# Kernel tuning notes

Measured on AMD Instinct MI355X. Metric: run time of the kernel, lower is better.

## Reference

```python
import jax, jax.numpy as jnp
import numpy as np

DIM = 512; HEADS = 8; DH = 64; INNER = HEADS * DH
GAMMA = 0.01; LREG = 1e-3
QB = 16; NS = 512


def _ln(x, g, b):
    mu = x.mean(-1, keepdims=True)
    var = jnp.var(x, axis=-1, keepdims=True)  # biased, matches torch LayerNorm
    return (x - mu) / jnp.sqrt(var + 1e-5) * g + b


def _std(x):
    return jnp.std(x, ddof=1)  # torch.std default is unbiased


def setup_inputs() -> dict:
    key = jax.random.key(0)
    ks = jax.random.split(key, 10)
    sc = lambda k, shape: (jax.random.normal(k, shape, jnp.float32) * 0.05)
    return {
        "q": jax.random.normal(ks[0], (QB, NS, DIM), jnp.float32),
        "k": jax.random.normal(ks[1], (QB, NS, DIM), jnp.float32),
        "v": jax.random.normal(ks[2], (QB, NS, DIM), jnp.float32),
        "ln1_g": jnp.ones((DIM,), jnp.float32),
        "ln1_b": jnp.zeros((DIM,), jnp.float32),
        "W_in": sc(ks[3], (DIM, INNER)),
        "wp_w1": sc(ks[4], (2 * DH, 2 * DH)),
        "wp_b1": jnp.zeros((2 * DH,), jnp.float32),
        "wp_ln_g": jnp.ones((2 * DH,), jnp.float32),
        "wp_ln_b": jnp.zeros((2 * DH,), jnp.float32),
        "wp_w2": sc(ks[5], (2 * DH, DH)),
        "wp_b2": jnp.zeros((DH,), jnp.float32),
        "wp_w3": sc(ks[6], (DH, 3)),
        "wp_b3": jnp.zeros((3,), jnp.float32),
        "weight_temp": jnp.array([0.5], jnp.float32),
        "W_out": sc(ks[7], (INNER, DIM)),
        "b_out": jnp.zeros((DIM,), jnp.float32),
    }


def _forward(q, k, v, ln1_g, ln1_b, W_in, wp_w1, wp_b1, wp_ln_g, wp_ln_b,
             wp_w2, wp_b2, wp_w3, wp_b3, weight_temp, W_out, b_out):
    eps = 1e-6

    def proj(t):  # LayerNorm -> Linear(no bias) -> [h, q, n, d]
        y = _ln(t, ln1_g, ln1_b) @ W_in
        Qb, Nb, _ = y.shape
        return y.reshape(Qb, Nb, HEADS, DH).transpose(2, 0, 1, 3)

    f_q, f_k, f_v = proj(q), proj(k), proj(v)
    m = f_k.shape[2]

    # --- cosine distance component ---
    dots_raw = jnp.einsum('hqnd,hqmd->hqnm', f_q, f_k)
    n1 = jnp.linalg.norm(f_q, axis=-1, keepdims=True) + eps          # [h,q,n,1]
    n2 = jnp.linalg.norm(f_k, axis=-1)[:, :, None, :] + eps          # [h,q,1,m]
    cosine_sim = jnp.clip(dots_raw / (n1 * n2), -0.9, 0.9)

    # --- regularized covariance component ---
    fkc = f_k - f_k.mean(axis=2, keepdims=True)   # center keys over n
    fqc = f_q - f_q.mean(axis=-1, keepdims=True)  # center queries over d
    cov = jnp.einsum('hqnd,hqmd->hqnm', fqc, fkc) / (DH ** 0.5 + 1e-6)
    cov = jnp.clip((LREG / max(m, 1)) * cov, -10.0, 10.0)

    # --- margin-based variance component (eval: adaptive_gamma = gamma) ---
    fqn = f_q / jnp.maximum(jnp.linalg.norm(f_q, axis=-1, keepdims=True), 1e-6)
    fkn = f_k / jnp.maximum(jnp.linalg.norm(f_k, axis=-1, keepdims=True), 1e-6)
    cs = jnp.clip(jnp.einsum('hqnd,hqmd->hqnm', fqn, fkn), -0.9, 0.9)
    margin = jnp.clip(GAMMA - cs, 0.0, 5.0)
    var_comp = jnp.broadcast_to(margin.mean(-1, keepdims=True), cs.shape)

    # --- dynamic per-head mixture weights ---
    feat = jnp.concatenate([f_q.mean((1, 2)), f_k.mean((1, 2))], axis=-1)  # [h, 2d]
    x = jax.nn.relu(_ln(feat @ wp_w1 + wp_b1, wp_ln_g, wp_ln_b))
    x = jax.nn.relu(x @ wp_w2 + wp_b2)
    wlog = jax.nn.softmax(x @ wp_w3 + wp_b3, axis=-1)  # predictor ends in Softmax
    wt = jnp.clip(weight_temp, 0.1, 2.0)
    w = jax.nn.softmax(wlog / wt, axis=-1)             # second softmax over temp
    w = jnp.clip(w, 0.05, 0.8)
    w = w / w.sum(-1, keepdims=True)
    cos_w = w[:, 0].reshape(HEADS, 1, 1, 1)
    cov_w = w[:, 1].reshape(HEADS, 1, 1, 1)
    var_w = w[:, 2].reshape(HEADS, 1, 1, 1)

    sg = jax.lax.stop_gradient  # norms are .detach()'d in torch
    dots = (cos_w * (cosine_sim / (sg(_std(cosine_sim)) + 1e-6))
            + cov_w * (cov / (sg(_std(cov)) + 1e-6) * 0.5)
            + var_w * (var_comp / (sg(_std(var_comp)) + 1e-6) * 0.5))

    ds = _std(dots)
    temp = jnp.where(ds < 1e-4, jnp.float32(0.1),
                     jnp.where(ds < 0.01, jnp.float32(0.3), 0.5 + ds))
    temp = jnp.clip(temp, 0.1, 3.0)

    attn = jax.nn.softmax(dots / temp, axis=-1)
    out = jnp.einsum('hqnm,hqmd->hqnd', attn, f_v)
    out = out.transpose(1, 2, 0, 3).reshape(q.shape[0], q.shape[1], INNER)
    return out @ W_out + b_out


def reference(q, k, v, ln1_g, ln1_b, W_in, wp_w1, wp_b1, wp_ln_g, wp_ln_b,
              wp_w2, wp_b2, wp_w3, wp_b3, weight_temp, W_out, b_out):
    return _forward(q, k, v, ln1_g, ln1_b, W_in, wp_w1, wp_b1, wp_ln_g,
                    wp_ln_b, wp_w2, wp_b2, wp_w3, wp_b3, weight_temp,
                    W_out, b_out)
```

## Files before the change

### kernel.cpp

```cpp
#include <hip/hip_runtime.h>
#include <math.h>

#define H 8
#define NS 512
#define D 64

typedef __bf16 bf16x8 __attribute__((ext_vector_type(8)));
typedef _Float16 f16x8 __attribute__((ext_vector_type(8)));
typedef float f32x4 __attribute__((ext_vector_type(4)));
typedef short s16x8 __attribute__((ext_vector_type(8)));
typedef short s16x4 __attribute__((ext_vector_type(4)));

#define CS2 ((1e-3f/512.f)/(8.f+1e-6f))
#define LOG2E 1.4426950408889634

static __device__ __forceinline__ f32x4 mfma16(bf16x8 a, bf16x8 b, f32x4 c){
  return __builtin_amdgcn_mfma_f32_16x16x32_bf16(a,b,c,0,0,0);
}
static __device__ __forceinline__ f32x4 mfma16h(f16x8 a, f16x8 b, f32x4 c){
  return __builtin_amdgcn_mfma_f32_16x16x32_f16(a,b,c,0,0,0);
}
static __device__ __forceinline__ float b2f(unsigned short s){
  union { unsigned u; float f; } v; v.u = ((unsigned)s)<<16; return v.f;
}
static __device__ __forceinline__ unsigned short f2b(float f){
  union { float f; unsigned u; } v; v.f = f;
  unsigned r = v.u + 0x7FFFu + ((v.u>>16)&1u);
  return (unsigned short)(r>>16);
}
static __device__ __forceinline__ unsigned short f2h(float f){
  union { _Float16 h; unsigned short s; } cv; cv.h = (_Float16)f; return cv.s;
}
static __device__ __forceinline__ float h2f(unsigned short s){
  union { _Float16 h; unsigned short s; } cv; cv.s = s; return (float)cv.h;
}
static __device__ __forceinline__ float wred64(float v){
  #pragma unroll
  for(int m=32; m>0; m>>=1) v += __shfl_xor(v, m, 64);
  return v;
}

constexpr size_t OFF_XNB = 0;
constexpr size_t OFF_FQB = 6291456;
constexpr size_t OFF_FKB = 8388608;
constexpr size_t OFF_FVB = 10485760;
constexpr size_t OFF_FVT = 12582912;
constexpr size_t OFF_WT  = 14680064;
constexpr size_t OFF_WOH = 14811136;
constexpr size_t OFF_WOL = 14942208;
constexpr size_t OFF_OHH = 15073280;
constexpr size_t OFF_ARR = 19267584;
constexpr size_t OFF_SMK = OFF_ARR + 9*65536;
constexpr size_t OFF_COEF= OFF_SMK + 128;
constexpr size_t OFF_DBL = OFF_COEF + 32;
constexpr size_t NDBL    = 72 + 1024;

__global__ __launch_bounds__(256) void k_pre(const float* __restrict__ q,
    const float* __restrict__ k, const float* __restrict__ v,
    const float* __restrict__ g, const float* __restrict__ b,
    const float* __restrict__ Win, const float* __restrict__ Wout,
    unsigned short* __restrict__ xnb, unsigned short* __restrict__ WT,
    unsigned short* __restrict__ WTh, unsigned short* __restrict__ WTl,
    double* __restrict__ dbl){
  int bx = blockIdx.x; int t = threadIdx.x;
  if(bx < 6144){
    int row = bx*4 + (t>>6); int l = t & 63;
    const float* src = (row < 8192) ? q : ((row < 16384) ? k : v);
    int r = row & 8191;
    const float4* sp = (const float4*)(src + (size_t)r*512);
    float4 v1 = sp[l*2], v2 = sp[l*2+1];
    float s  = v1.x+v1.y+v1.z+v1.w + v2.x+v2.y+v2.z+v2.w;
    float ss = v1.x*v1.x+v1.y*v1.y+v1.z*v1.z+v1.w*v1.w
             + v2.x*v2.x+v2.y*v2.y+v2.z*v2.z+v2.w*v2.w;
    s = wred64(s); ss = wred64(ss);
    float mu = s*(1.f/512.f);
    float var = ss*(1.f/512.f) - mu*mu;
    float rstd = rsqrtf(var + 1e-5f);
    const float4* gp = (const float4*)g; const float4* bp = (const float4*)b;
    float4 g1 = gp[l*2], g2 = gp[l*2+1], b1 = bp[l*2], b2 = bp[l*2+1];
    s16x8 o;
    o[0]=(short)f2b((v1.x-mu)*rstd*g1.x+b1.x); o[1]=(short)f2b((v1.y-mu)*rstd*g1.y+b1.y);
    o[2]=(short)f2b((v1.z-mu)*rstd*g1.z+b1.z); o[3]=(short)f2b((v1.w-mu)*rstd*g1.w+b1.w);
    o[4]=(short)f2b((v2.x-mu)*rstd*g2.x+b2.x); o[5]=(short)f2b((v2.y-mu)*rstd*g2.y+b2.y);
    o[6]=(short)f2b((v2.z-mu)*rstd*g2.z+b2.z); o[7]=(short)f2b((v2.w-mu)*rstd*g2.w+b2.w);
    *(s16x8*)(xnb + (size_t)row*512 + l*8) = o;
    return;
  }
  __shared__ float tile[64][65];
  if(bx < 6208){
    int bb = bx - 6144; int kt = bb>>3, nt = bb&7;
    if(bb==0){
      for(int i=t;i<(int)NDBL;i+=256) dbl[i]=0.0;
    }
    #pragma unroll
    for(int i=0;i<4;i++){
      int row = (t>>4) + i*16; int col = (t&15)*4;
      float4 vv = *(const float4*)(Win + (size_t)(kt*64+row)*512 + nt*64 + col);
      tile[row][col]=vv.x; tile[row][col+1]=vv.y; tile[row][col+2]=vv.z; tile[row][col+3]=vv.w;
    }
    __syncthreads();
    #pragma unroll
    for(int i=0;i<4;i++){
      int n = (t>>4) + i*16; int ck = (t&15)*4;
      s16x4 o;
      #pragma unroll
      for(int j=0;j<4;j++) o[j] = (short)f2b(tile[ck+j][n]);
      *(s16x4*)(WT + (size_t)(nt*64+n)*512 + kt*64 + ck) = o;
    }
  } else {
    int bb = bx - 6208; int kt = bb>>3, nt = bb&7;
    #pragma unroll
    for(int i=0;i<4;i++){
      int row = (t>>4) + i*16; int col = (t&15)*4;
      float4 vv = *(const float4*)(Wout + (size_t)(kt*64+row)*512 + nt*64 + col);
      tile[row][col]=vv.x; tile[row][col+1]=vv.y; tile[row][col+2]=vv.z; tile[row][col+3]=vv.w;
    }
    __syncthreads();
    #pragma unroll
    for(int i=0;i<4;i++){
      int n = (t>>4) + i*16; int ck = (t&15)*4;
      s16x4 oh_, ol_;
      #pragma unroll
      for(int j=0;j<4;j++){
        float x = tile[ck+j][n];
        unsigned short hi = f2h(x);
        oh_[j] = (short)hi;
        ol_[j] = (short)f2h(x - h2f(hi));
      }
      *(s16x4*)(WTh + (size_t)(nt*64+n)*512 + kt*64 + ck) = oh_;
      *(s16x4*)(WTl + (size_t)(nt*64+n)*512 + kt*64 + ck) = ol_;
    }
  }
}

__global__ __launch_bounds__(256) void k_mm1(const unsigned short* __restrict__ xnb,
    const unsigned short* __restrict__ WT,
    unsigned short* __restrict__ fqb, unsigned short* __restrict__ fkb,
    unsigned short* __restrict__ fvb){
  __shared__ __align__(16) unsigned short As[128*64];
  __shared__ __align__(16) unsigned short Bs[128*64];
  int t = threadIdx.x; int w = t>>6; int l = t&63; int g = l>>4, lc = l&15;
  int bid = blockIdx.x;
  int work = (bid&7)*96 + (bid>>3);
  int Rb = (work>>2)*128, cb = (work&3)*128;
  int wr = (w>>1)*64, wc = (w&1)*64;
  f32x4 acc[4][4];
  #pragma unroll
  for(int i=0;i<4;i++)
    #pragma unroll
    for(int j=0;j<4;j++) acc[i][j] = (f32x4){0.f,0.f,0.f,0.f};
  for(int k0=0; k0<512; k0+=64){
    __syncthreads();
    #pragma unroll
    for(int i=0;i<4;i++){
      int c = t + i*256; int row = c>>3, k8 = c&7;
      s16x8 va = *(const s16x8*)(xnb + (size_t)(Rb+row)*512 + k0 + k8*8);
      *(s16x8*)((char*)As + row*128 + ((k8*16) ^ ((row&7)<<4))) = va;
      s16x8 vb = *(const s16x8*)(WT + (size_t)(cb+row)*512 + k0 + k8*8);
      *(s16x8*)((char*)Bs + row*128 + ((k8*16) ^ ((row&7)<<4))) = vb;
    }
    __syncthreads();
    #pragma unroll
    for(int ks=0; ks<2; ks++){
      bf16x8 ar[4], br[4];
      #pragma unroll
      for(int rt=0; rt<4; rt++){
        int row = wr + rt*16 + lc;
        ar[rt] = *(const bf16x8*)((const char*)As + row*128 + (((ks*4+g)*16) ^ ((row&7)<<4)));
      }
      #pragma unroll
      for(int ct=0; ct<4; ct++){
        int row = wc + ct*16 + lc;
        br[ct] = *(const bf16x8*)((const char*)Bs + row*128 + (((ks*4+g)*16) ^ ((row&7)<<4)));
      }
      #pragma unroll
      for(int rt=0; rt<4; rt++)
        #pragma unroll
        for(int ct=0; ct<4; ct++)
          acc[rt][ct] = mfma16(ar[rt], br[ct], acc[rt][ct]);
    }
  }
  #pragma unroll
  for(int rt=0; rt<4; rt++){
    #pragma unroll
    for(int r=0; r<4; r++){
      int R = Rb + wr + rt*16 + g*4 + r;
      int tsel = R>>13; int rr = R&8191;
      unsigned short* dst = (tsel==0)?fqb:((tsel==1)?fkb:fvb);
      #pragma unroll
      for(int ct=0; ct<4; ct++){
        int c = cb + wc + ct*16 + lc;
        dst[(size_t)rr*512 + c] = f2b(acc[rt][ct][r]);
      }
    }
  }
}

__global__ __launch_bounds__(512) void k_mid(const unsigned short* __restrict__ fqb,
    const unsigned short* __restrict__ fkb, const unsigned short* __restrict__ fvb,
    float* __restrict__ smk, double* featd,
    float* __restrict__ ri1, float* __restrict__ mq, float* __restrict__ qdm,
    float* __restrict__ ri2, float* __restrict__ sk,
    unsigned short* __restrict__ fvT){
  int bx = blockIdx.x; int t = threadIdx.x;
  if(bx < 128){
    int hq = bx; int h = hq>>4, q = hq&15;
    __shared__ float cq[8][64], ck[8][64], mkS[64];
    __shared__ float smkS;
    {
      int d = t&63; int g = t>>6;
      float aq=0.f, ak=0.f;
      for(int n=g; n<512; n+=8){
        size_t base = (size_t)(q*512+n)*512 + h*64 + d;
        aq += b2f(fqb[base]);
        ak += b2f(fkb[base]);
      }
      cq[g][d]=aq; ck[g][d]=ak;
    }
    __syncthreads();
    if(t<64){
      float sq=0.f, sk2=0.f;
      #pragma unroll
      for(int i=0;i<8;i++){ sq+=cq[i][t]; sk2+=ck[i][t]; }
      atomicAdd(&featd[h*128+t], (double)sq);
      atomicAdd(&featd[h*128+64+t], (double)sk2);
      float mk = sk2*(1.f/512.f);
      mkS[t]=mk;
      float s = wred64(mk);
      if(t==0){ smk[hq]=s; smkS=s; }
    }
    __syncthreads();
    {
      int n = t;
      float smkv = smkS;
      const unsigned short* fr = fqb + (size_t)(q*512+n)*512 + h*64;
      const unsigned short* kr = fkb + (size_t)(q*512+n)*512 + h*64;
      float sq=0.f, ssq=0.f, dq=0.f, sks=0.f, ssk=0.f;
      #pragma unroll
      for(int j=0;j<8;j++){
        s16x8 vq = *(const s16x8*)(fr + j*8);
        s16x8 vk = *(const s16x8*)(kr + j*8);
        #pragma unroll
        for(int e=0;e<8;e++){
          float a = b2f((unsigned short)vq[e]);
          float c = b2f((unsigned short)vk[e]);
          sq += a; ssq += a*a; dq += a*mkS[j*8+e];
          sks += c; ssk += c*c;
        }
      }
      int idx = hq*512 + n;
      float nq = sqrtf(ssq);
      ri1[idx]  = 1.f/(nq+1e-6f);
      mq[idx]   = sq*(1.f/64.f);
      qdm[idx]  = dq;
      float nk = sqrtf(ssk);
      ri2[idx]  = 1.f/(nk+1e-6f);
      sk[idx]   = sks - smkv;
    }
    return;
  }
  {
    int bb = bx - 128; int hq = bb>>2, nc = bb&3;
    int h = hq>>4, q = hq&15; int n0 = nc*128;
    __shared__ float tile[128][65];
    #pragma unroll
    for(int i=0;i<2;i++){
      int c = t + i*512; int row = c>>3, k8 = c&7;
      s16x8 v = *(const s16x8*)(fvb + (size_t)(q*512 + n0 + row)*512 + h*64 + k8*8);
      #pragma unroll
      for(int j=0;j<8;j++) tile[row][k8*8+j] = b2f((unsigned short)v[j]);
    }
    __syncthreads();
    #pragma unroll
    for(int i=0;i<2;i++){
      int c = t + i*512; int d = c>>4, n8 = c&15;
      s16x8 o;
      #pragma unroll
      for(int j=0;j<8;j++){
        int p = n8*8+j;
        int pl = p & 31;
        int src = (p & ~31) | (16*(pl&1) + (pl>>1));
        o[j] = (short)f2h(tile[src][d]);
      }
      *(s16x8*)(fvT + (size_t)(hq*64 + d)*512 + n0 + n8*8) = o;
    }
  }
}

__global__ __launch_bounds__(512) void k_comp(const unsigned short* __restrict__ fqb,
    const unsigned short* __restrict__ fkb,
    const float* __restrict__ ri1,
    const float* __restrict__ mq, const float* __restrict__ qdm,
    const float* __restrict__ ri2,
    const float* __restrict__ skp,
    float* __restrict__ mxcg, float* __restrict__ mxvg, double* headsum){
  int bid = blockIdx.x;
  int bx = (bid&7)*64 + (bid>>3);
  int hq = bx>>2; int rt = bx&3;
  int h = hq>>4, q = hq&15; int n0 = rt*128;
  __shared__ __align__(16) unsigned short Qs[128*64];
  __shared__ __align__(16) unsigned short Ks[128*64];
  __shared__ float ri2f[512], skf[512];
  __shared__ float red[8][9];
  int t = threadIdx.x; int w = t>>6; int l = t&63; int g = l>>4, lc = l&15;
  for(int i=t; i<512; i+=512){
    ri2f[i]=ri2[hq*NS+i]; skf[i]=skp[hq*NS+i];
  }
  #pragma unroll
  for(int i=0;i<2;i++){
    int c = t + i*512; int row = c>>3, k8 = c&7;
    s16x8 v = *(const s16x8*)(fqb + (size_t)(q*512 + n0 + row)*512 + h*64 + k8*8);
    *(s16x8*)((char*)Qs + row*128 + ((k8*16) ^ ((row&7)<<4))) = v;
  }
  float ri1r[4], mqr[4], qdmr[4];
  #pragma unroll
  for(int r=0;r<4;r++){
    int n = hq*NS + n0 + w*16 + g*4 + r;
    ri1r[r]=ri1[n]; mqr[r]=mq[n]; qdmr[r]=qdm[n];
  }
  __syncthreads();
  bf16x8 aq[2];
  #pragma unroll
  for(int ks=0;ks<2;ks++){
    int row = 16*w + lc;
    aq[ks] = *(const bf16x8*)((const char*)Qs + row*128 + (((ks*4+g)*16) ^ ((row&7)<<4)));
  }
  float p1=0,p3=0,p4=0;
  float rm_m[4]={0,0,0,0}, rm_c[4]={0,0,0,0}, rm_v[4]={0,0,0,0};
  float mxc[4]={-1e30f,-1e30f,-1e30f,-1e30f}, mxv[4]={-1e30f,-1e30f,-1e30f,-1e30f};
  for(int mc=0; mc<4; mc++){
    __syncthreads();
    #pragma unroll
    for(int i=0;i<2;i++){
      int c = t + i*512; int row = c>>3, k8 = c&7;
      s16x8 v = *(const s16x8*)(fkb + (size_t)(q*512 + mc*128 + row)*512 + h*64 + k8*8);
      *(s16x8*)((char*)Ks + row*128 + ((k8*16) ^ ((row&7)<<4))) = v;
    }
    __syncthreads();
    #pragma unroll 2
    for(int mt=0; mt<8; mt++){
      f32x4 dacc = (f32x4){0.f,0.f,0.f,0.f};
      #pragma unroll
      for(int ks=0;ks<2;ks++){
        int row = mt*16 + lc;
        bf16x8 bk = *(const bf16x8*)((const char*)Ks + row*128 + (((ks*4+g)*16) ^ ((row&7)<<4)));
        dacc = mfma16(aq[ks], bk, dacc);
      }
      int m = mc*128 + mt*16 + lc;
      float r2 = ri2f[m], sc = skf[m];
      #pragma unroll
      for(int r=0;r<4;r++){
        float dv = dacc[r];
        float cosv = fminf(fmaxf(dv*ri1r[r]*r2, -0.9f), 0.9f);
        float inner = (dv - qdmr[r]) - mqr[r]*sc;
        float marg = fmaxf(0.01f - cosv, 0.f);
        p1 += cosv*cosv; p3 += inner*inner; p4 += cosv*inner;
        rm_m[r]+=marg; rm_c[r]+=cosv; rm_v[r]+=inner;
        mxc[r]=fmaxf(mxc[r],cosv); mxv[r]=fmaxf(mxv[r],inner);
      }
    }
  }
  float p0 = rm_c[0]+rm_c[1]+rm_c[2]+rm_c[3];
  float p2 = rm_v[0]+rm_v[1]+rm_v[2]+rm_v[3];
  #pragma unroll
  for(int off=1; off<16; off<<=1){
    #pragma unroll
    for(int r=0;r<4;r++){
      rm_m[r]+=__shfl_xor(rm_m[r],off,64);
      rm_c[r]+=__shfl_xor(rm_c[r],off,64);
      rm_v[r]+=__shfl_xor(rm_v[r],off,64);
      mxc[r]=fmaxf(mxc[r],__shfl_xor(mxc[r],off,64));
      mxv[r]=fmaxf(mxv[r],__shfl_xor(mxv[r],off,64));
    }
  }
  float q0=0,q1=0,q2=0,q3=0;
  if(lc==0){
    #pragma unroll
    for(int r=0;r<4;r++){
      float vmv = rm_m[r]*(1.f/512.f);
      q0+=vmv; q1+=vmv*vmv; q2+=vmv*rm_c[r]; q3+=vmv*rm_v[r];
      int n = n0 + w*16 + g*4 + r;
      mxcg[hq*NS+n]=mxc[r]; mxvg[hq*NS+n]=mxv[r];
    }
  }
  float all9[9] = {p0,p1,p2,p3,p4,q0,q1,q2,q3};
  #pragma unroll
  for(int j=0;j<9;j++){
    float vv = wred64(all9[j]);
    if(l==0) red[w][j]=vv;
  }
  __syncthreads();
  if(t<9){
    double s = 0.0;
    #pragma unroll
    for(int i=0;i<8;i++) s += (double)red[i][t];
    atomicAdd(&headsum[h*9+t], s);
  }
}

__global__ __launch_bounds__(512) void k_finalize(const double* headsum, const double* featd,
    const float* __restrict__ w1, const float* __restrict__ b1,
    const float* __restrict__ lng, const float* __restrict__ lnb,
    const float* __restrict__ w2, const float* __restrict__ b2,
    const float* __restrict__ w3, const float* __restrict__ b3,
    const float* __restrict__ wtemp, float* coef){
  __shared__ float fS[1024];
  __shared__ float x1[1024];
  __shared__ float x2[512];
  __shared__ float oS[8][3], whS[8][3];
  int t = threadIdx.x;
  fS[t]     = (float)(featd[t]     * (1.0/8192.0));
  fS[t+512] = (float)(featd[t+512] * (1.0/8192.0));
  __syncthreads();
  int hh = t>>6, j = t&63;
  {
    float a0 = b1[j], a1 = b1[j+64];
    #pragma unroll 8
    for(int i=0;i<128;i++){
      float f = fS[hh*128+i];
      a0 += f*w1[(size_t)i*128 + j];
      a1 += f*w1[(size_t)i*128 + j + 64];
    }
    float s = a0+a1, ss = a0*a0+a1*a1;
    s = wred64(s); ss = wred64(ss);
    float mu = s*(1.f/128.f), var = ss*(1.f/128.f)-mu*mu;
    float rstd = rsqrtf(var+1e-5f);
    x1[hh*128+j]    = fmaxf((a0-mu)*rstd*lng[j]+lnb[j], 0.f);
    x1[hh*128+j+64] = fmaxf((a1-mu)*rstd*lng[j+64]+lnb[j+64], 0.f);
  }
  __syncthreads();
  {
    float s2 = b2[j];
    #pragma unroll 8
    for(int i=0;i<128;i++) s2 += x1[hh*128+i]*w2[(size_t)i*64+j];
    x2[hh*64+j] = fmaxf(s2, 0.f);
  }
  __syncthreads();
  if(t < 24){
    int h3 = t/3, j3 = t-h3*3;
    float s3=0.f;
    #pragma unroll 8
    for(int i=0;i<64;i++) s3 += x2[h3*64+i]*w3[i*3+j3];
    oS[h3][j3] = s3 + b3[j3];
  }
  __syncthreads();
  if(t < 8){
    float o0=oS[t][0], o1=oS[t][1], o2=oS[t][2];
    float mx=fmaxf(o0,fmaxf(o1,o2));
    float e0=expf(o0-mx), e1=expf(o1-mx), e2=expf(o2-mx), se=e0+e1+e2;
    float l0=e0/se, l1=e1/se, l2=e2/se;
    float wt=fminf(fmaxf(wtemp[0],0.1f),2.0f);
    l0/=wt; l1/=wt; l2/=wt;
    mx=fmaxf(l0,fmaxf(l1,l2));
    e0=expf(l0-mx); e1=expf(l1-mx); e2=expf(l2-mx); se=e0+e1+e2;
    float u0=fminf(fmaxf(e0/se,0.05f),0.8f);
    float u1=fminf(fmaxf(e1/se,0.05f),0.8f);
    float u2=fminf(fmaxf(e2/se,0.05f),0.8f);
    float su=u0+u1+u2;
    whS[t][0]=u0/su; whS[t][1]=u1/su; whS[t][2]=u2/su;
  }
  __syncthreads();
  if(t==0){
    const double N = 33554432.0;
    const double CS2d = (double)CS2;
    double gs[9];
    for(int jj=0;jj<9;jj++){ double s=0; for(int h2=0;h2<8;h2++) s+=headsum[h2*9+jj]; gs[jj]=s; }
    auto sd = [&](double s, double ss)->double{
      double vv=(ss - s*s/N)/(N-1.0); return vv>0.0 ? sqrt(vv) : 0.0;
    };
    double std_cos = sd(gs[0],gs[1]);
    double std_cov = sd(CS2d*gs[2], CS2d*CS2d*gs[3]);
    double std_vm  = sd(512.0*gs[5], 512.0*gs[6]);
    double sdot=0.0, sdot2=0.0;
    double Af[8], Bf[8];
    for(int h2=0;h2<8;h2++){
      const double* hs = headsum + h2*9;
      double A = (double)whS[h2][0]/(std_cos+1e-6);
      double Bi = (double)whS[h2][1]/(std_cov+1e-6)*0.5*CS2d;
      double C = (double)whS[h2][2]/(std_vm +1e-6)*0.5;
      sdot  += A*hs[0] + Bi*hs[2] + C*512.0*hs[5];
      sdot2 += A*A*hs[1] + Bi*Bi*hs[3] + C*C*512.0*hs[6]
             + 2.0*A*Bi*hs[4] + 2.0*A*C*hs[7] + 2.0*Bi*C*hs[8];
      Af[h2]=A; Bf[h2]=Bi;
    }
    double dstd = sd(sdot, sdot2);
    double temp = dstd < 1e-4 ? 0.1 : (dstd < 0.01 ? 0.3 : 0.5 + dstd);
    temp = fmin(fmax(temp, 0.1), 3.0);
    for(int h2=0;h2<8;h2++){
      coef[h2]   = (float)(Af[h2]/temp*LOG2E);
      coef[8+h2] = (float)(Bf[h2]/temp*LOG2E);
    }
    coef[16] = (float)temp;
  }
}

__global__ __launch_bounds__(512) void k_flash(const unsigned short* __restrict__ fqb,
    const unsigned short* __restrict__ fkb, const unsigned short* __restrict__ fvT,
    const float* __restrict__ ri1, const float* __restrict__ mq,
    const float* __restrict__ qdm, const float* __restrict__ ri2,
    const float* __restrict__ skp,
    const float* __restrict__ mxcg, const float* __restrict__ mxvg,
    const float* __restrict__ coef,
    unsigned short* __restrict__ ohh){
  int bid = blockIdx.x;
  int bx = (bid&7)*64 + (bid>>3);
  int hq = bx>>2; int rt = bx&3;
  int h = hq>>4, q = hq&15; int n0 = rt*128;
  __shared__ __align__(16) unsigned short Qs[128*64];
  __shared__ __align__(16) unsigned short Ks[128*64];
  __shared__ __align__(16) unsigned short Vt[64*128];
  __shared__ float ri2f[512], skf[512];
  int t = threadIdx.x; int w = t>>6; int l = t&63; int g = l>>4, lc = l&15;
  for(int i=t; i<512; i+=512){ ri2f[i]=ri2[hq*NS+i]; skf[i]=skp[hq*NS+i]; }
  #pragma unroll
  for(int i=0;i<2;i++){
    int c = t + i*512; int row = c>>3, k8 = c&7;
    s16x8 v = *(const s16x8*)(fqb + (size_t)(q*512 + n0 + row)*512 + h*64 + k8*8);
    *(s16x8*)((char*)Qs + row*128 + ((k8*16) ^ ((row&7)<<4))) = v;
  }
  float Ah = coef[h], Bh = coef[8+h];
  float loA = -0.9f*Ah, hiA = 0.9f*Ah;
  float ri1A[4], R1[4], R2[4];
  #pragma unroll
  for(int r=0;r<4;r++){
    int n = hq*NS + n0 + w*16 + g*4 + r;
    float Mr = Ah*mxcg[n] + Bh*mxvg[n];
    ri1A[r] = ri1[n]*Ah;
    R1[r] = fmaf(Bh, qdm[n], Mr);
    R2[r] = Bh*mq[n];
  }
  __syncthreads();
  bf16x8 aq[2];
  #pragma unroll
  for(int ks=0;ks<2;ks++){
    int row = 16*w + lc;
    aq[ks] = *(const bf16x8*)((const char*)Qs + row*128 + (((ks*4+g)*16) ^ ((row&7)<<4)));
  }
  f32x4 acc[4];
  #pragma unroll
  for(int dt=0;dt<4;dt++) acc[dt] = (f32x4){0.f,0.f,0.f,0.f};
  float lsum[4]={0.f,0.f,0.f,0.f};
  unsigned short* Pw = Qs + w*640;
  unsigned* Pu = (unsigned*)Pw;
  for(int mc=0; mc<4; mc++){
    __syncthreads();
    #pragma unroll
    for(int i=0;i<2;i++){
      int c = t + i*512; int row = c>>3, k8 = c&7;
      s16x8 v = *(const s16x8*)(fkb + (size_t)(q*512 + mc*128 + row)*512 + h*64 + k8*8);
      *(s16x8*)((char*)Ks + row*128 + ((k8*16) ^ ((row&7)<<4))) = v;
    }
    #pragma unroll
    for(int i=0;i<2;i++){
      int c = t + i*512; int d = c>>4, m8 = c&15;
      s16x8 v = *(const s16x8*)(fvT + (size_t)(hq*64 + d)*512 + mc*128 + m8*8);
      *(s16x8*)((char*)Vt + d*256 + ((m8*16) ^ ((d&7)<<4))) = v;
    }
    __syncthreads();
    #pragma unroll 1
    for(int mt2=0; mt2<4; mt2++){
      f32x4 d0 = (f32x4){0.f,0.f,0.f,0.f};
      f32x4 d1 = (f32x4){0.f,0.f,0.f,0.f};
      #pragma unroll
      for(int ks=0;ks<2;ks++){
        int row0 = (mt2*2)*16 + lc;
        bf16x8 bk0 = *(const bf16x8*)((const char*)Ks + row0*128 + (((ks*4+g)*16) ^ ((row0&7)<<4)));
        d0 = mfma16(aq[ks], bk0, d0);
        int row1 = (mt2*2+1)*16 + lc;
        bf16x8 bk1 = *(const bf16x8*)((const char*)Ks + row1*128 + (((ks*4+g)*16) ^ ((row1&7)<<4)));
        d1 = mfma16(aq[ks], bk1, d1);
      }
      int m0 = mc*128 + mt2*32 + lc;
      float r20 = ri2f[m0],    sc0 = skf[m0];
      float r21 = ri2f[m0+16], sc1 = skf[m0+16];
      #pragma unroll
      for(int r=0;r<4;r++){
        float dv0 = d0[r], dv1 = d1[r];
        float cl0 = fminf(fmaxf(dv0*ri1A[r]*r20, loA), hiA);
        float cl1 = fminf(fmaxf(dv1*ri1A[r]*r21, loA), hiA);
        float e0 = fmaf(-R2[r], sc0, fmaf(Bh, dv0, -R1[r]));
        float e1 = fmaf(-R2[r], sc1, fmaf(Bh, dv1, -R1[r]));
        float pe0 = __builtin_amdgcn_exp2f(cl0 + e0);
        float pe1 = __builtin_amdgcn_exp2f(cl1 + e1);
        lsum[r] += pe0 + pe1;
        auto ph = __builtin_amdgcn_cvt_pkrtz(pe0, pe1);
        unsigned pk; __builtin_memcpy(&pk, &ph, 4);
        Pu[(g*4+r)*20 + lc] = pk;
      }
      asm volatile("s_waitcnt lgkmcnt(0)" ::: "memory");
      f16x8 ap = *(const f16x8*)((const char*)Pw + lc*80 + g*16);
      #pragma unroll
      for(int dt=0;dt<4;dt++){
        int drow = dt*16 + lc;
        f16x8 bv = *(const f16x8*)((const char*)Vt + drow*256 + (((mt2*4+g)*16) ^ ((drow&7)<<4)));
        acc[dt] = mfma16h(ap, bv, acc[dt]);
      }
    }
  }
  #pragma unroll
  for(int off=1; off<16; off<<=1){
    #pragma unroll
    for(int r=0;r<4;r++) lsum[r] += __shfl_xor(lsum[r], off, 64);
  }
  #pragma unroll
  for(int r=0;r<4;r++){
    float inv = 1.f/lsum[r];
    int n = n0 + w*16 + g*4 + r;
    #pragma unroll
    for(int dt=0;dt<4;dt++){
      size_t idx = (size_t)(q*512 + n)*512 + h*64 + dt*16 + lc;
      ohh[idx] = f2h(acc[dt][r]*inv);
    }
  }
}

__global__ __launch_bounds__(256) void k_gout2(const unsigned short* __restrict__ Ap,
    const unsigned short* __restrict__ Bhp, const unsigned short* __restrict__ Blp,
    const float* __restrict__ bias, float* __restrict__ Cout){
  __shared__ __align__(16) unsigned short As[128*64];
  __shared__ __align__(16) unsigned short BsH[128*64];
  __shared__ __align__(16) unsigned short BsL[128*64];
  int t = threadIdx.x; int w = t>>6; int l = t&63; int g = l>>4, lc = l&15;
  int bid = blockIdx.x;
  int work = (bid&7)*32 + (bid>>3);
  int Rb = (work>>2)*128, cb = (work&3)*128;
  int wr = (w>>1)*64, wc = (w&1)*64;
  f32x4 acc[4][4];
  #pragma unroll
  for(int i=0;i<4;i++)
    #pragma unroll
    for(int j=0;j<4;j++) acc[i][j] = (f32x4){0.f,0.f,0.f,0.f};
  for(int k0=0; k0<512; k0+=64){
    __syncthreads();
    #pragma unroll
    for(int i=0;i<4;i++){
      int c = t + i*256; int row = c>>3, k8 = c&7;
      int sw = (k8*16) ^ ((row&7)<<4);
      *(s16x8*)((char*)As  + row*128 + sw) = *(const s16x8*)(Ap  + (size_t)(Rb+row)*512 + k0 + k8*8);
      *(s16x8*)((char*)BsH + row*128 + sw) = *(const s16x8*)(Bhp + (size_t)(cb+row)*512 + k0 + k8*8);
      *(s16x8*)((char*)BsL + row*128 + sw) = *(const s16x8*)(Blp + (size_t)(cb+row)*512 + k0 + k8*8);
    }
    __syncthreads();
    #pragma unroll
    for(int ks=0; ks<2; ks++){
      f16x8 ar[4], brh[4], brl[4];
      #pragma unroll
      for(int rt=0; rt<4; rt++){
        int row = wr + rt*16 + lc;
        ar[rt] = *(const f16x8*)((const char*)As + row*128 + (((ks*4+g)*16) ^ ((row&7)<<4)));
      }
      #pragma unroll
      for(int ct=0; ct<4; ct++){
        int row = wc + ct*16 + lc;
        int off = row*128 + (((ks*4+g)*16) ^ ((row&7)<<4));
        brh[ct] = *(const f16x8*)((const char*)BsH + off);
        brl[ct] = *(const f16x8*)((const char*)BsL + off);
      }
      #pragma unroll
      for(int rt=0; rt<4; rt++)
        #pragma unroll
        for(int ct=0; ct<4; ct++){
          acc[rt][ct] = mfma16h(ar[rt], brh[ct], acc[rt][ct]);
          acc[rt][ct] = mfma16h(ar[rt], brl[ct], acc[rt][ct]);
        }
    }
  }
  #pragma unroll
  for(int rt=0; rt<4; rt++){
    #pragma unroll
    for(int r=0; r<4; r++){
      int R = Rb + wr + rt*16 + g*4 + r;
      #pragma unroll
      for(int ct=0; ct<4; ct++){
        int c = cb + wc + ct*16 + lc;
        Cout[(size_t)R*512 + c] = acc[rt][ct][r] + bias[c];
      }
    }
  }
}

extern "C" void kernel_launch(void* const* d_in, const int* in_sizes, int n_in,
                              void* d_out, int out_size, void* d_ws, size_t ws_size,
                              hipStream_t stream){
  const float* q    = (const float*)d_in[0];
  const float* k    = (const float*)d_in[1];
  const float* v    = (const float*)d_in[2];
  const float* ln1g = (const float*)d_in[3];
  const float* ln1b = (const float*)d_in[4];
  const float* Win  = (const float*)d_in[5];
  const float* w1   = (const float*)d_in[6];
  const float* b1   = (const float*)d_in[7];
  const float* lng  = (const float*)d_in[8];
  const float* lnb  = (const float*)d_in[9];
  const float* w2   = (const float*)d_in[10];
  const float* b2   = (const float*)d_in[11];
  const float* w3   = (const float*)d_in[12];
  const float* b3   = (const float*)d_in[13];
  const float* wtemp= (const float*)d_in[14];
  const float* Wout = (const float*)d_in[15];
  const float* bout = (const float*)d_in[16];

  float* w = (float*)d_ws;
  unsigned short* xnb = (unsigned short*)(w + OFF_XNB);
  unsigned short* fqb = (unsigned short*)(w + OFF_FQB);
  unsigned short* fkb = (unsigned short*)(w + OFF_FKB);
  unsigned short* fvb = (unsigned short*)(w + OFF_FVB);
  unsigned short* fvT = (unsigned short*)(w + OFF_FVT);
  unsigned short* wtb = (unsigned short*)(w + OFF_WT);
  unsigned short* woh = (unsigned short*)(w + OFF_WOH);
  unsigned short* wol = (unsigned short*)(w + OFF_WOL);
  unsigned short* ohh = (unsigned short*)(w + OFF_OHH);
  float* ri1  = w + OFF_ARR + 0*65536;
  float* mq_  = w + OFF_ARR + 2*65536;
  float* qdm  = w + OFF_ARR + 3*65536;
  float* ri2  = w + OFF_ARR + 4*65536;
  float* sk_  = w + OFF_ARR + 6*65536;
  float* mxc  = w + OFF_ARR + 7*65536;
  float* mxv  = w + OFF_ARR + 8*65536;
  float* smk_ = w + OFF_SMK;
  float* coef = w + OFF_COEF;
  double* dbl = (double*)(w + OFF_DBL);
  double* headsum = dbl;
  double* featd   = dbl + 72;

  k_pre<<<6272, 256, 0, stream>>>(q, k, v, ln1g, ln1b, Win, Wout, xnb, wtb, woh, wol, dbl);
  k_mm1<<<768, 256, 0, stream>>>(xnb, wtb, fqb, fkb, fvb);
  k_mid<<<640, 512, 0, stream>>>(fqb, fkb, fvb, smk_, featd, ri1, mq_, qdm, ri2, sk_, fvT);
  k_comp<<<512, 512, 0, stream>>>(fqb, fkb, ri1, mq_, qdm, ri2, sk_, mxc, mxv, headsum);
  k_finalize<<<1, 512, 0, stream>>>(headsum, featd, w1, b1, lng, lnb, w2, b2, w3, b3, wtemp, coef);
  k_flash<<<512, 512, 0, stream>>>(fqb, fkb, fvT, ri1, mq_, qdm, ri2, sk_, mxc, mxv, coef, ohh);
  k_gout2<<<256, 256, 0, stream>>>(ohh, woh, wol, bout, (float*)d_out);
}
```

Measured before the change: 143.5 us.

## Fuse input LayerNorm into projection GEMM prologue, drop bf16 normalized buffer

Moves the LayerNorm of q/k/v out of the preprocessing kernel and into the projection GEMM. Each GEMM block first computes per-row mean and rstd for its 128 rows, then normalizes and converts fp32 inputs to bf16 while filling the A tile in shared memory. This removes the write and re-read of the 24576x512 bf16 intermediate and shrinks k_pre to only the weight transposes. In exchange, each row of fp32 input is now read several times (a stats pass plus once per column block) at twice the bytes of bf16, and the stats pass sits on the critical path before the MFMA loop.

```diff
diff --git a/kernel.cpp b/kernel.cpp
--- a/kernel.cpp
+++ b/kernel.cpp
@@ -40,7 +40,6 @@
   return v;
 }
 
-constexpr size_t OFF_XNB = 0;
 constexpr size_t OFF_FQB = 6291456;
 constexpr size_t OFF_FKB = 8388608;
 constexpr size_t OFF_FVB = 10485760;
@@ -55,41 +54,15 @@
 constexpr size_t OFF_DBL = OFF_COEF + 32;
 constexpr size_t NDBL    = 72 + 1024;
 
-__global__ __launch_bounds__(256) void k_pre(const float* __restrict__ q,
-    const float* __restrict__ k, const float* __restrict__ v,
-    const float* __restrict__ g, const float* __restrict__ b,
-    const float* __restrict__ Win, const float* __restrict__ Wout,
-    unsigned short* __restrict__ xnb, unsigned short* __restrict__ WT,
+__global__ __launch_bounds__(256) void k_pre(const float* __restrict__ Win, const float* __restrict__ Wout,
+    unsigned short* __restrict__ WT,
     unsigned short* __restrict__ WTh, unsigned short* __restrict__ WTl,
     double* __restrict__ dbl){
   int bx = blockIdx.x; int t = threadIdx.x;
-  if(bx < 6144){
-    int row = bx*4 + (t>>6); int l = t & 63;
-    const float* src = (row < 8192) ? q : ((row < 16384) ? k : v);
-    int r = row & 8191;
-    const float4* sp = (const float4*)(src + (size_t)r*512);
-    float4 v1 = sp[l*2], v2 = sp[l*2+1];
-    float s  = v1.x+v1.y+v1.z+v1.w + v2.x+v2.y+v2.z+v2.w;
-    float ss = v1.x*v1.x+v1.y*v1.y+v1.z*v1.z+v1.w*v1.w
-             + v2.x*v2.x+v2.y*v2.y+v2.z*v2.z+v2.w*v2.w;
-    s = wred64(s); ss = wred64(ss);
-    float mu = s*(1.f/512.f);
-    float var = ss*(1.f/512.f) - mu*mu;
-    float rstd = rsqrtf(var + 1e-5f);
-    const float4* gp = (const float4*)g; const float4* bp = (const float4*)b;
-    float4 g1 = gp[l*2], g2 = gp[l*2+1], b1 = bp[l*2], b2 = bp[l*2+1];
-    s16x8 o;
-    o[0]=(short)f2b((v1.x-mu)*rstd*g1.x+b1.x); o[1]=(short)f2b((v1.y-mu)*rstd*g1.y+b1.y);
-    o[2]=(short)f2b((v1.z-mu)*rstd*g1.z+b1.z); o[3]=(short)f2b((v1.w-mu)*rstd*g1.w+b1.w);
-    o[4]=(short)f2b((v2.x-mu)*rstd*g2.x+b2.x); o[5]=(short)f2b((v2.y-mu)*rstd*g2.y+b2.y);
-    o[6]=(short)f2b((v2.z-mu)*rstd*g2.z+b2.z); o[7]=(short)f2b((v2.w-mu)*rstd*g2.w+b2.w);
-    *(s16x8*)(xnb + (size_t)row*512 + l*8) = o;
-    return;
-  }
   __shared__ float tile[64][65];
-  if(bx < 6208){
-    int bb = bx - 6144; int kt = bb>>3, nt = bb&7;
-    if(bb==0){
+  if(bx < 64){
+    int kt = bx>>3, nt = bx&7;
+    if(bx==0){
       for(int i=t;i<(int)NDBL;i+=256) dbl[i]=0.0;
     }
     #pragma unroll
@@ -108,7 +81,7 @@
       *(s16x4*)(WT + (size_t)(nt*64+n)*512 + kt*64 + ck) = o;
     }
   } else {
-    int bb = bx - 6208; int kt = bb>>3, nt = bb&7;
+    int bb = bx - 64; int kt = bb>>3, nt = bb&7;
     #pragma unroll
     for(int i=0;i<4;i++){
       int row = (t>>4) + i*16; int col = (t&15)*4;
@@ -133,29 +106,69 @@
   }
 }
 
-__global__ __launch_bounds__(256) void k_mm1(const unsigned short* __restrict__ xnb,
+__global__ __launch_bounds__(256) void k_mm1(const float* __restrict__ q,
+    const float* __restrict__ k, const float* __restrict__ v,
+    const float* __restrict__ g, const float* __restrict__ b,
     const unsigned short* __restrict__ WT,
     unsigned short* __restrict__ fqb, unsigned short* __restrict__ fkb,
     unsigned short* __restrict__ fvb){
   __shared__ __align__(16) unsigned short As[128*64];
   __shared__ __align__(16) unsigned short Bs[128*64];
-  int t = threadIdx.x; int w = t>>6; int l = t&63; int g = l>>4, lc = l&15;
+  __shared__ float muS[128], rsS[128];
+  __shared__ float gS[512], bS[512];
+  int t = threadIdx.x; int w = t>>6; int l = t&63; int g2 = l>>4, lc = l&15;
   int bid = blockIdx.x;
   int work = (bid&7)*96 + (bid>>3);
   int Rb = (work>>2)*128, cb = (work&3)*128;
+  int tsel = Rb>>13;
+  const float* src = (tsel==0)?q:((tsel==1)?k:v);
+  int r0 = Rb & 8191;
+  unsigned short* dst = (tsel==0)?fqb:((tsel==1)?fkb:fvb);
   int wr = (w>>1)*64, wc = (w&1)*64;
+  for(int i=t;i<512;i+=256){ gS[i]=g[i]; bS[i]=b[i]; }
+  {
+    int r = t>>1, p = t&1;
+    const float4* rp = (const float4*)(src + (size_t)(r0+r)*512) + p*64;
+    float s=0.f, ss=0.f;
+    #pragma unroll 8
+    for(int i=0;i<64;i++){
+      float4 x = rp[i];
+      s  += x.x+x.y+x.z+x.w;
+      ss += x.x*x.x+x.y*x.y+x.z*x.z+x.w*x.w;
+    }
+    s += __shfl_xor(s,1,64); ss += __shfl_xor(ss,1,64);
+    if(p==0){
+      float mu = s*(1.f/512.f);
+      float var = ss*(1.f/512.f) - mu*mu;
+      muS[r] = mu; rsS[r] = rsqrtf(var + 1e-5f);
+    }
+  }
   f32x4 acc[4][4];
   #pragma unroll
   for(int i=0;i<4;i++)
     #pragma unroll
     for(int j=0;j<4;j++) acc[i][j] = (f32x4){0.f,0.f,0.f,0.f};
+  __syncthreads();
   for(int k0=0; k0<512; k0+=64){
-    __syncthreads();
+    if(k0) __syncthreads();
     #pragma unroll
     for(int i=0;i<4;i++){
       int c = t + i*256; int row = c>>3, k8 = c&7;
-      s16x8 va = *(const s16x8*)(xnb + (size_t)(Rb+row)*512 + k0 + k8*8);
-      *(s16x8*)((char*)As + row*128 + ((k8*16) ^ ((row&7)<<4))) = va;
+      const float* ap = src + (size_t)(r0+row)*512 + k0 + k8*8;
+      float4 x0 = *(const float4*)ap;
+      float4 x1 = *(const float4*)(ap+4);
+      float mu = muS[row], rs = rsS[row];
+      int cg = k0 + k8*8;
+      s16x8 o;
+      o[0]=(short)f2b((x0.x-mu)*rs*gS[cg+0]+bS[cg+0]);
+      o[1]=(short)f2b((x0.y-mu)*rs*gS[cg+1]+bS[cg+1]);
+      o[2]=(short)f2b((x0.z-mu)*rs*gS[cg+2]+bS[cg+2]);
+      o[3]=(short)f2b((x0.w-mu)*rs*gS[cg+3]+bS[cg+3]);
+      o[4]=(short)f2b((x1.x-mu)*rs*gS[cg+4]+bS[cg+4]);
+      o[5]=(short)f2b((x1.y-mu)*rs*gS[cg+5]+bS[cg+5]);
+      o[6]=(short)f2b((x1.z-mu)*rs*gS[cg+6]+bS[cg+6]);
+      o[7]=(short)f2b((x1.w-mu)*rs*gS[cg+7]+bS[cg+7]);
+      *(s16x8*)((char*)As + row*128 + ((k8*16) ^ ((row&7)<<4))) = o;
       s16x8 vb = *(const s16x8*)(WT + (size_t)(cb+row)*512 + k0 + k8*8);
       *(s16x8*)((char*)Bs + row*128 + ((k8*16) ^ ((row&7)<<4))) = vb;
     }
@@ -166,12 +179,12 @@
       #pragma unroll
       for(int rt=0; rt<4; rt++){
         int row = wr + rt*16 + lc;
-        ar[rt] = *(const bf16x8*)((const char*)As + row*128 + (((ks*4+g)*16) ^ ((row&7)<<4)));
+        ar[rt] = *(const bf16x8*)((const char*)As + row*128 + (((ks*4+g2)*16) ^ ((row&7)<<4)));
       }
       #pragma unroll
       for(int ct=0; ct<4; ct++){
         int row = wc + ct*16 + lc;
-        br[ct] = *(const bf16x8*)((const char*)Bs + row*128 + (((ks*4+g)*16) ^ ((row&7)<<4)));
+        br[ct] = *(const bf16x8*)((const char*)Bs + row*128 + (((ks*4+g2)*16) ^ ((row&7)<<4)));
       }
       #pragma unroll
       for(int rt=0; rt<4; rt++)
@@ -184,9 +197,7 @@
   for(int rt=0; rt<4; rt++){
     #pragma unroll
     for(int r=0; r<4; r++){
-      int R = Rb + wr + rt*16 + g*4 + r;
-      int tsel = R>>13; int rr = R&8191;
-      unsigned short* dst = (tsel==0)?fqb:((tsel==1)?fkb:fvb);
+      int rr = r0 + wr + rt*16 + g2*4 + r;
       #pragma unroll
       for(int ct=0; ct<4; ct++){
         int c = cb + wc + ct*16 + lc;
@@ -701,7 +712,6 @@
   const float* bout = (const float*)d_in[16];
 
   float* w = (float*)d_ws;
-  unsigned short* xnb = (unsigned short*)(w + OFF_XNB);
   unsigned short* fqb = (unsigned short*)(w + OFF_FQB);
   unsigned short* fkb = (unsigned short*)(w + OFF_FKB);
   unsigned short* fvb = (unsigned short*)(w + OFF_FVB);
@@ -723,8 +733,8 @@
   double* headsum = dbl;
   double* featd   = dbl + 72;
 
-  k_pre<<<6272, 256, 0, stream>>>(q, k, v, ln1g, ln1b, Win, Wout, xnb, wtb, woh, wol, dbl);
-  k_mm1<<<768, 256, 0, stream>>>(xnb, wtb, fqb, fkb, fvb);
+  k_pre<<<128, 256, 0, stream>>>(Win, Wout, wtb, woh, wol, dbl);
+  k_mm1<<<768, 256, 0, stream>>>(q, k, v, ln1g, ln1b, wtb, fqb, fkb, fvb);
   k_mid<<<640, 512, 0, stream>>>(fqb, fkb, fvb, smk_, featd, ri1, mq_, qdm, ri2, sk_, fvT);
   k_comp<<<512, 512, 0, stream>>>(fqb, fkb, ri1, mq_, qdm, ri2, sk_, mxc, mxv, headsum);
   k_finalize<<<1, 512, 0, stream>>>(headsum, featd, w1, b1, lng, lnb, w2, b2, w3, b3, wtemp, coef);
```

Measured after the change: 181.3 us. 1.26x slower.
